# Optimization experiments

Hardware: AMD Instinct MI355X
Metric: run time of the kernel (lower is better)

Reference implementation:

```python
import jax, jax.numpy as jnp
import numpy as np

D_MODEL = 512
N_HEADS = 8
D_K = D_MODEL // N_HEADS  # 64
MAX_LEN = 5000


def _positional_encoding(d_model, max_len):
    pe = np.zeros((max_len, d_model), dtype=np.float32)
    position = np.arange(max_len, dtype=np.float32)[:, None]
    div_term = np.exp(np.arange(0, d_model, 2, dtype=np.float32) * (-np.log(10000.0) / d_model))
    pe[:, 0::2] = np.sin(position * div_term)
    pe[:, 1::2] = np.cos(position * div_term)
    return jnp.asarray(pe)


def _layer_norm(x, gamma, beta, eps):
    mu = jnp.mean(x, axis=-1, keepdims=True)
    var = jnp.mean(jnp.square(x - mu), axis=-1, keepdims=True)
    return (x - mu) * jax.lax.rsqrt(var + eps) * gamma + beta


def setup_inputs() -> dict:
    key = jax.random.key(0)
    ks = jax.random.split(key, 5)
    s = 1.0 / np.sqrt(D_MODEL)
    return {
        "x": jax.random.normal(ks[0], (4, 2048, D_MODEL), dtype=jnp.float32),
        "ln1_g": jnp.ones((D_MODEL,), jnp.float32),
        "ln1_b": jnp.zeros((D_MODEL,), jnp.float32),
        "wq": jax.random.normal(ks[1], (D_MODEL, D_MODEL), jnp.float32) * s,
        "wk": jax.random.normal(ks[2], (D_MODEL, D_MODEL), jnp.float32) * s,
        "wv": jax.random.normal(ks[3], (D_MODEL, D_MODEL), jnp.float32) * s,
        "wfc": jax.random.normal(ks[4], (D_MODEL, D_MODEL), jnp.float32) * s,
        "ln2_g": jnp.ones((D_MODEL,), jnp.float32),
        "ln2_b": jnp.zeros((D_MODEL,), jnp.float32),
    }


def reference(x, ln1_g, ln1_b, wq, wk, wv, wfc, ln2_g, ln2_b):
    B, T, D = x.shape
    residual0 = x
    # outer pre-norm (nn.LayerNorm default eps=1e-5)
    h = _layer_norm(x, ln1_g, ln1_b, 1e-5)
    # sinusoidal positional encoding
    h = h + _positional_encoding(D_MODEL, MAX_LEN)[:T]
    residual1 = h
    # projections -> [B, H, T, d]
    q = (h @ wq).reshape(B, T, N_HEADS, D_K).transpose(0, 2, 1, 3)
    k = (h @ wk).reshape(B, T, N_HEADS, D_K).transpose(0, 2, 1, 3)
    v = (h @ wv).reshape(B, T, N_HEADS, D_K).transpose(0, 2, 1, 3)
    scale = 1.0 / np.sqrt(D_K).astype(np.float32)
    attn = jnp.einsum("bhqd,bhkd->bhqk", q * scale, k)
    causal = jnp.tril(jnp.ones((T, T), dtype=bool))  # subsequent mask
    attn = jnp.where(causal, attn, jnp.float32(-1e9))
    attn = jax.nn.softmax(attn, axis=-1)
    o = jnp.einsum("bhqk,bhkd->bhqd", attn, v)
    o = o.transpose(0, 2, 1, 3).reshape(B, T, D)
    o = o @ wfc
    # inner post-attention residual + LayerNorm (eps=1e-6)
    h2 = _layer_norm(o + residual1, ln2_g, ln2_b, 1e-6)
    return h2 + residual0
```

## Files before the change

kernel.cpp:

```cpp
#include <hip/hip_runtime.h>
#include <hip/hip_bf16.h>

#define B_ 4
#define T_ 2048
#define D_ 512

typedef __attribute__((ext_vector_type(8))) short short8;
typedef __attribute__((ext_vector_type(4))) short short4v;
typedef __attribute__((ext_vector_type(4))) float float4v;
typedef unsigned short bf16_t;

__device__ __forceinline__ bf16_t f2bf(float f) {
  unsigned int u = __builtin_bit_cast(unsigned int, f);
  unsigned int r = (u + 0x7fffu + ((u >> 16) & 1u)) >> 16;
  return (bf16_t)r;
}

__device__ __forceinline__ float waveReduceSum(float v) {
#pragma unroll
  for (int m = 32; m >= 1; m >>= 1) v += __shfl_xor(v, m, 64);
  return v;
}

__device__ __forceinline__ void gld16(const bf16_t* g, bf16_t* l) {
  __builtin_amdgcn_global_load_lds(
      (const __attribute__((address_space(1))) void*)g,
      (__attribute__((address_space(3))) void*)l, 16, 0, 0);
}

__global__ __launch_bounds__(256) void wconv_kernel(
    const float* __restrict__ wq, const float* __restrict__ wk,
    const float* __restrict__ wv, const float* __restrict__ wfc,
    bf16_t* __restrict__ wqkvT, bf16_t* __restrict__ wfcT) {
  for (int idx = blockIdx.x * 256 + threadIdx.x; idx < 1048576; idx += 262144) {
    if (idx < 786432) {
      int n = idx >> 9, k = idx & 511;
      const float* src = (n < 512) ? wq : ((n < 1024) ? wk : wv);
      float scl = (n >= 512 && n < 1024) ? 0.125f : 1.0f;
      int c = n & 511;
      wqkvT[idx] = f2bf(src[k * 512 + c] * scl);
    } else {
      int j = idx - 786432;
      int n = j >> 9, k = j & 511;
      wfcT[j] = f2bf(wfc[k * 512 + n]);
    }
  }
}

__global__ __launch_bounds__(256) void ln1_pe_kernel(
    const float* __restrict__ x, const float* __restrict__ g,
    const float* __restrict__ bb, float* __restrict__ h_f32,
    bf16_t* __restrict__ h_bf16) {
  int wave = threadIdx.x >> 6, lane = threadIdx.x & 63;
  int row = blockIdx.x * 4 + wave;
  int pos = row & (T_ - 1);
  const float* xr = x + (size_t)row * D_;
  int c0 = lane * 8;
  float v[8];
  float4 a = *(const float4*)(xr + c0);
  float4 b4 = *(const float4*)(xr + c0 + 4);
  v[0]=a.x; v[1]=a.y; v[2]=a.z; v[3]=a.w;
  v[4]=b4.x; v[5]=b4.y; v[6]=b4.z; v[7]=b4.w;
  float s = 0.f;
#pragma unroll
  for (int j = 0; j < 8; ++j) s += v[j];
  s = waveReduceSum(s);
  float mu = s * (1.f / 512.f);
  float q = 0.f;
#pragma unroll
  for (int j = 0; j < 8; ++j) { float d = v[j] - mu; q += d * d; }
  q = waveReduceSum(q);
  float rstd = rsqrtf(q * (1.f / 512.f) + 1e-5f);
  float* hr = h_f32 + (size_t)row * D_;
  bf16_t* hb = h_bf16 + (size_t)row * D_;
#pragma unroll
  for (int j = 0; j < 8; ++j) {
    int col = c0 + j;
    float hn = (v[j] - mu) * rstd * g[col] + bb[col];
    int i2 = (col >> 1) << 1;
    float dt = __expf((float)i2 * (-9.2103403719761836f / 512.0f));
    float ang = (float)pos * dt;
    float pe = (col & 1) ? __cosf(ang) : __sinf(ang);
    float hv = hn + pe;
    hr[col] = hv;
    hb[col] = f2bf(hv);
  }
}

template <int N_COLS, int OUT_BF16>
__global__ __launch_bounds__(256) void gemm128_kernel(
    const bf16_t* __restrict__ A, const bf16_t* __restrict__ Bt,
    void* __restrict__ Cv) {
  __shared__ __align__(16) bf16_t As[128 * 64];
  __shared__ __align__(16) bf16_t Bs[128 * 64];
  const int m0 = blockIdx.y * 128, n0 = blockIdx.x * 128;
  const int tid = threadIdx.x;
  const int w = tid >> 6, lane = tid & 63;
  const int ln = lane & 15, quad = lane >> 4;
  const int wy = w >> 1, wx = w & 1;
  const int sw = ln & 7;

  float4v acc[4][4];
  float4v z = {0.f, 0.f, 0.f, 0.f};
#pragma unroll
  for (int i = 0; i < 4; ++i)
#pragma unroll
    for (int j = 0; j < 4; ++j) acc[i][j] = z;

  for (int k0 = 0; k0 < 512; k0 += 64) {
#pragma unroll
    for (int i = 0; i < 4; ++i) {
      int cbase = w * 256 + i * 64;
      int chunk = cbase + lane;
      int row = chunk >> 3;
      int lb = (chunk & 7) ^ (row & 7);
      gld16(A + (size_t)(m0 + row) * 512 + k0 + lb * 8, As + (size_t)cbase * 8);
      gld16(Bt + (size_t)(n0 + row) * 512 + k0 + lb * 8, Bs + (size_t)cbase * 8);
    }
    __syncthreads();
#pragma unroll
    for (int c = 0; c < 2; ++c) {
      short8 af[4], bf[4];
#pragma unroll
      for (int mt = 0; mt < 4; ++mt) {
        int row = wy * 64 + mt * 16 + ln;
        int pb = (c * 4 + quad) ^ sw;
        af[mt] = *(const short8*)(As + row * 64 + pb * 8);
      }
#pragma unroll
      for (int nt = 0; nt < 4; ++nt) {
        int row = wx * 64 + nt * 16 + ln;
        int pb = (c * 4 + quad) ^ sw;
        bf[nt] = *(const short8*)(Bs + row * 64 + pb * 8);
      }
#pragma unroll
      for (int mt = 0; mt < 4; ++mt)
#pragma unroll
        for (int nt = 0; nt < 4; ++nt)
          acc[mt][nt] = __builtin_amdgcn_mfma_f32_16x16x32_bf16(af[mt], bf[nt], acc[mt][nt], 0, 0, 0);
    }
    __syncthreads();
  }
#pragma unroll
  for (int mt = 0; mt < 4; ++mt)
#pragma unroll
    for (int r = 0; r < 4; ++r) {
      int row = m0 + wy * 64 + mt * 16 + quad * 4 + r;
#pragma unroll
      for (int nt = 0; nt < 4; ++nt) {
        int col = n0 + wx * 64 + nt * 16 + ln;
        if (OUT_BF16)
          ((bf16_t*)Cv)[(size_t)row * N_COLS + col] = f2bf(acc[mt][nt][r]);
        else
          ((float*)Cv)[(size_t)row * N_COLS + col] = acc[mt][nt][r];
      }
    }
}

__global__ __launch_bounds__(256) void attn_kernel(const bf16_t* __restrict__ qk,
                                                   const bf16_t* __restrict__ vT,
                                                   bf16_t* __restrict__ out) {
  __shared__ __align__(16) bf16_t Ks[2][64 * 64];
  __shared__ __align__(16) bf16_t Vs[2][64 * 64];
  __shared__ __align__(16) bf16_t Ps[4][16 * 72];
  const int bx = blockIdx.x;
  const int qt = 31 - (bx >> 5);
  const int bh = bx & 31;
  const int b = bh >> 3, h = bh & 7;
  const int tid = threadIdx.x;
  const int w = tid >> 6, lane = tid & 63;
  const int ln = lane & 15, quad = lane >> 4;
  const int sw = ln & 7;

  short8 qf0, qf1;
  {
    size_t qrow = ((size_t)b * T_ + qt * 64 + w * 16 + ln) * 1024 + h * 64;
    qf0 = *(const short8*)(qk + qrow + quad * 8);
    qf1 = *(const short8*)(qk + qrow + 32 + quad * 8);
  }
  float4v z = {0.f, 0.f, 0.f, 0.f};
  float4v oacc[4];
#pragma unroll
  for (int i = 0; i < 4; ++i) oacc[i] = z;
  float m_s = -1e30f, l_s = 0.f;

  const bf16_t* kbase = qk + (size_t)b * T_ * 1024 + 512 + h * 64;
  const bf16_t* vbase = vT + (size_t)(h * 64) * 8192 + (size_t)b * T_;
  bf16_t* Psw = Ps[w];

  auto stage = [&](int buf, int kt) {
#pragma unroll
    for (int i = 0; i < 2; ++i) {
      int cbase = w * 128 + i * 64;
      int chunk = cbase + lane;
      int row = chunk >> 3;
      int lb = (chunk & 7) ^ (row & 7);
      gld16(kbase + (size_t)(kt * 64 + row) * 1024 + lb * 8, Ks[buf] + (size_t)cbase * 8);
      gld16(vbase + (size_t)row * 8192 + kt * 64 + lb * 8, Vs[buf] + (size_t)cbase * 8);
    }
  };

  auto compute = [&](const bf16_t* Kc, const bf16_t* Vc, bool mask) {
    float sv[4][4];
#pragma unroll
    for (int mt = 0; mt < 4; ++mt) {
      float4v st = z;
      int row = mt * 16 + ln;
      short8 a0 = *(const short8*)(Kc + row * 64 + ((0 + quad) ^ sw) * 8);
      short8 a1 = *(const short8*)(Kc + row * 64 + ((4 + quad) ^ sw) * 8);
      st = __builtin_amdgcn_mfma_f32_16x16x32_bf16(a0, qf0, st, 0, 0, 0);
      st = __builtin_amdgcn_mfma_f32_16x16x32_bf16(a1, qf1, st, 0, 0, 0);
#pragma unroll
      for (int r = 0; r < 4; ++r) {
        float v = st[r];
        if (mask) {
          int kloc = mt * 16 + quad * 4 + r;
          if (kloc > w * 16 + ln) v = -1e30f;
        }
        sv[mt][r] = v;
      }
    }
    float mx = sv[0][0];
#pragma unroll
    for (int mt = 0; mt < 4; ++mt)
#pragma unroll
      for (int r = 0; r < 4; ++r) mx = fmaxf(mx, sv[mt][r]);
    mx = fmaxf(mx, __shfl_xor(mx, 16, 64));
    mx = fmaxf(mx, __shfl_xor(mx, 32, 64));
    float mn = fmaxf(m_s, mx);
    float alpha = __expf(m_s - mn);
    m_s = mn;
    float rs = 0.f;
#pragma unroll
    for (int mt = 0; mt < 4; ++mt)
#pragma unroll
      for (int r = 0; r < 4; ++r) {
        float p = __expf(sv[mt][r] - mn);
        sv[mt][r] = p;
        rs += p;
      }
    rs += __shfl_xor(rs, 16, 64);
    rs += __shfl_xor(rs, 32, 64);
    l_s = l_s * alpha + rs;
#pragma unroll
    for (int dt = 0; dt < 4; ++dt)
#pragma unroll
      for (int r = 0; r < 4; ++r) oacc[dt][r] *= alpha;
#pragma unroll
    for (int mt = 0; mt < 4; ++mt) {
      short4v p4;
#pragma unroll
      for (int r = 0; r < 4; ++r) p4[r] = (short)f2bf(sv[mt][r]);
      *(short4v*)(Psw + ln * 72 + mt * 16 + quad * 4) = p4;
    }
    short8 bp0 = *(short8*)(Psw + ln * 72 + quad * 8);
    short8 bp1 = *(short8*)(Psw + ln * 72 + 32 + quad * 8);
#pragma unroll
    for (int dt = 0; dt < 4; ++dt) {
      int row = dt * 16 + ln;
      short8 av0 = *(const short8*)(Vc + row * 64 + ((0 + quad) ^ sw) * 8);
      short8 av1 = *(const short8*)(Vc + row * 64 + ((4 + quad) ^ sw) * 8);
      oacc[dt] = __builtin_amdgcn_mfma_f32_16x16x32_bf16(av0, bp0, oacc[dt], 0, 0, 0);
      oacc[dt] = __builtin_amdgcn_mfma_f32_16x16x32_bf16(av1, bp1, oacc[dt], 0, 0, 0);
    }
  };

  stage(0, 0);
  __syncthreads();
  for (int kt = 0; kt < qt; ++kt) {
    int cur = kt & 1;
    stage(cur ^ 1, kt + 1);
    compute(Ks[cur], Vs[cur], false);
    __syncthreads();
  }
  compute(Ks[qt & 1], Vs[qt & 1], true);

  float inv = 1.0f / l_s;
  size_t obase = ((size_t)b * T_ + qt * 64 + w * 16 + ln) * 512 + h * 64;
#pragma unroll
  for (int dt = 0; dt < 4; ++dt) {
    short4v o4;
#pragma unroll
    for (int r = 0; r < 4; ++r) o4[r] = (short)f2bf(oacc[dt][r] * inv);
    *(short4v*)(out + obase + dt * 16 + quad * 4) = o4;
  }
}

__global__ __launch_bounds__(256) void ln2_kernel(
    const float* __restrict__ o2, const float* __restrict__ hres,
    const float* __restrict__ x, const float* __restrict__ g,
    const float* __restrict__ bb, float* __restrict__ out) {
  int wave = threadIdx.x >> 6, lane = threadIdx.x & 63;
  int row = blockIdx.x * 4 + wave;
  size_t ro = (size_t)row * D_;
  int c0 = lane * 8;
  float t[8];
  float4 a0 = *(const float4*)(o2 + ro + c0);
  float4 a1 = *(const float4*)(o2 + ro + c0 + 4);
  float4 h0 = *(const float4*)(hres + ro + c0);
  float4 h1 = *(const float4*)(hres + ro + c0 + 4);
  t[0]=a0.x+h0.x; t[1]=a0.y+h0.y; t[2]=a0.z+h0.z; t[3]=a0.w+h0.w;
  t[4]=a1.x+h1.x; t[5]=a1.y+h1.y; t[6]=a1.z+h1.z; t[7]=a1.w+h1.w;
  float s = 0.f;
#pragma unroll
  for (int j = 0; j < 8; ++j) s += t[j];
  s = waveReduceSum(s);
  float mu = s * (1.f / 512.f);
  float q = 0.f;
#pragma unroll
  for (int j = 0; j < 8; ++j) { float d = t[j] - mu; q += d * d; }
  q = waveReduceSum(q);
  float rstd = rsqrtf(q * (1.f / 512.f) + 1e-6f);
#pragma unroll
  for (int j = 0; j < 8; ++j) {
    int col = c0 + j;
    out[ro + col] = (t[j] - mu) * rstd * g[col] + bb[col] + x[ro + col];
  }
}

extern "C" void kernel_launch(void* const* d_in, const int* in_sizes, int n_in,
                              void* d_out, int out_size, void* d_ws, size_t ws_size,
                              hipStream_t stream) {
  const float* x   = (const float*)d_in[0];
  const float* g1  = (const float*)d_in[1];
  const float* b1  = (const float*)d_in[2];
  const float* wq  = (const float*)d_in[3];
  const float* wk  = (const float*)d_in[4];
  const float* wv  = (const float*)d_in[5];
  const float* wfc = (const float*)d_in[6];
  const float* g2  = (const float*)d_in[7];
  const float* b2  = (const float*)d_in[8];
  float* out = (float*)d_out;

  char* ws = (char*)d_ws;
  const size_t O_HF32  = 0;
  const size_t O_HBF   = 16777216;
  const size_t O_WQKV  = 25165824;
  const size_t O_WFC   = 26738688;
  const size_t O_QK    = 27262976;
  const size_t O_VT    = 44040192;
  const size_t O_ATTN  = 52428800;
  const size_t O_O2    = 60817408;
  const size_t WS_NEED = 77594624;
  if (ws_size < WS_NEED) return;

  float*  h_f32 = (float*)(ws + O_HF32);
  bf16_t* h_bf  = (bf16_t*)(ws + O_HBF);
  bf16_t* wqkvT = (bf16_t*)(ws + O_WQKV);
  bf16_t* wfcT  = (bf16_t*)(ws + O_WFC);
  bf16_t* qk    = (bf16_t*)(ws + O_QK);
  bf16_t* vT    = (bf16_t*)(ws + O_VT);
  bf16_t* attn  = (bf16_t*)(ws + O_ATTN);
  float*  o2    = (float*)(ws + O_O2);

  wconv_kernel<<<dim3(1024), dim3(256), 0, stream>>>(wq, wk, wv, wfc, wqkvT, wfcT);
  ln1_pe_kernel<<<dim3(2048), dim3(256), 0, stream>>>(x, g1, b1, h_f32, h_bf);
  gemm128_kernel<1024, 1><<<dim3(8, 64), dim3(256), 0, stream>>>(h_bf, wqkvT, (void*)qk);
  gemm128_kernel<8192, 1><<<dim3(64, 4), dim3(256), 0, stream>>>(wqkvT + 1024 * 512, h_bf, (void*)vT);
  attn_kernel<<<dim3(1024), dim3(256), 0, stream>>>(qk, vT, attn);
  gemm128_kernel<512, 0><<<dim3(4, 64), dim3(256), 0, stream>>>(attn, wfcT, (void*)o2);
  ln2_kernel<<<dim3(2048), dim3(256), 0, stream>>>(o2, h_f32, x, g2, b2, out);
}
```

Measured before the change: 196.9 us.

## Fuse prep kernels, double-buffer GEMMs, merge QKV launches, fold residual into GEMM epilogue

Result: no change. 196.0 us (-0.5%).

```diff
diff --git a/kernel.cpp b/kernel.cpp
--- a/kernel.cpp
+++ b/kernel.cpp
@@ -15,6 +15,10 @@
   unsigned int r = (u + 0x7fffu + ((u >> 16) & 1u)) >> 16;
   return (bf16_t)r;
 }
+__device__ __forceinline__ float bf2f(bf16_t b) {
+  unsigned int u = ((unsigned int)b) << 16;
+  return __builtin_bit_cast(float, u);
+}
 
 __device__ __forceinline__ float waveReduceSum(float v) {
 #pragma unroll
@@ -28,29 +32,32 @@
       (__attribute__((address_space(3))) void*)l, 16, 0, 0);
 }
 
-__global__ __launch_bounds__(256) void wconv_kernel(
+__global__ __launch_bounds__(256) void pre_kernel(
+    const float* __restrict__ x, const float* __restrict__ g,
+    const float* __restrict__ bb,
     const float* __restrict__ wq, const float* __restrict__ wk,
     const float* __restrict__ wv, const float* __restrict__ wfc,
+    bf16_t* __restrict__ h_bf16,
     bf16_t* __restrict__ wqkvT, bf16_t* __restrict__ wfcT) {
-  for (int idx = blockIdx.x * 256 + threadIdx.x; idx < 1048576; idx += 262144) {
-    if (idx < 786432) {
-      int n = idx >> 9, k = idx & 511;
-      const float* src = (n < 512) ? wq : ((n < 1024) ? wk : wv);
-      float scl = (n >= 512 && n < 1024) ? 0.125f : 1.0f;
-      int c = n & 511;
-      wqkvT[idx] = f2bf(src[k * 512 + c] * scl);
-    } else {
-      int j = idx - 786432;
-      int n = j >> 9, k = j & 511;
-      wfcT[j] = f2bf(wfc[k * 512 + n]);
-    }
-  }
-}
-
-__global__ __launch_bounds__(256) void ln1_pe_kernel(
-    const float* __restrict__ x, const float* __restrict__ g,
-    const float* __restrict__ bb, float* __restrict__ h_f32,
-    bf16_t* __restrict__ h_bf16) {
+  if (blockIdx.x >= 2048) {
+    int bid = blockIdx.x - 2048;
+#pragma unroll 4
+    for (int i = 0; i < 16; ++i) {
+      int idx = bid * 4096 + i * 256 + threadIdx.x;
+      if (idx < 786432) {
+        int n = idx >> 9, k = idx & 511;
+        const float* src = (n < 512) ? wq : ((n < 1024) ? wk : wv);
+        float scl = (n >= 512 && n < 1024) ? 0.125f : 1.0f;
+        int c = n & 511;
+        wqkvT[idx] = f2bf(src[k * 512 + c] * scl);
+      } else {
+        int j = idx - 786432;
+        int n = j >> 9, k = j & 511;
+        wfcT[j] = f2bf(wfc[k * 512 + n]);
+      }
+    }
+    return;
+  }
   int wave = threadIdx.x >> 6, lane = threadIdx.x & 63;
   int row = blockIdx.x * 4 + wave;
   int pos = row & (T_ - 1);
@@ -71,7 +78,6 @@
   for (int j = 0; j < 8; ++j) { float d = v[j] - mu; q += d * d; }
   q = waveReduceSum(q);
   float rstd = rsqrtf(q * (1.f / 512.f) + 1e-5f);
-  float* hr = h_f32 + (size_t)row * D_;
   bf16_t* hb = h_bf16 + (size_t)row * D_;
 #pragma unroll
   for (int j = 0; j < 8; ++j) {
@@ -81,19 +87,15 @@
     float dt = __expf((float)i2 * (-9.2103403719761836f / 512.0f));
     float ang = (float)pos * dt;
     float pe = (col & 1) ? __cosf(ang) : __sinf(ang);
-    float hv = hn + pe;
-    hr[col] = hv;
-    hb[col] = f2bf(hv);
-  }
-}
-
-template <int N_COLS, int OUT_BF16>
-__global__ __launch_bounds__(256) void gemm128_kernel(
-    const bf16_t* __restrict__ A, const bf16_t* __restrict__ Bt,
-    void* __restrict__ Cv) {
-  __shared__ __align__(16) bf16_t As[128 * 64];
-  __shared__ __align__(16) bf16_t Bs[128 * 64];
-  const int m0 = blockIdx.y * 128, n0 = blockIdx.x * 128;
+    hb[col] = f2bf(hn + pe);
+  }
+}
+
+template <typename EPI>
+__device__ __forceinline__ void gemm_body(const bf16_t* __restrict__ A,
+                                          const bf16_t* __restrict__ Bt,
+                                          int m0, int n0, bf16_t* As, bf16_t* Bs,
+                                          EPI epi) {
   const int tid = threadIdx.x;
   const int w = tid >> 6, lane = tid & 63;
   const int ln = lane & 15, quad = lane >> 4;
@@ -107,32 +109,34 @@
 #pragma unroll
     for (int j = 0; j < 4; ++j) acc[i][j] = z;
 
-  for (int k0 = 0; k0 < 512; k0 += 64) {
+  auto stage = [&](int buf, int k0) {
 #pragma unroll
     for (int i = 0; i < 4; ++i) {
       int cbase = w * 256 + i * 64;
       int chunk = cbase + lane;
       int row = chunk >> 3;
       int lb = (chunk & 7) ^ (row & 7);
-      gld16(A + (size_t)(m0 + row) * 512 + k0 + lb * 8, As + (size_t)cbase * 8);
-      gld16(Bt + (size_t)(n0 + row) * 512 + k0 + lb * 8, Bs + (size_t)cbase * 8);
-    }
-    __syncthreads();
+      gld16(A + (size_t)(m0 + row) * 512 + k0 + lb * 8, As + buf * 8192 + cbase * 8);
+      gld16(Bt + (size_t)(n0 + row) * 512 + k0 + lb * 8, Bs + buf * 8192 + cbase * 8);
+    }
+  };
+
+  stage(0, 0);
+  __syncthreads();
+  for (int kb = 0; kb < 8; ++kb) {
+    int cur = kb & 1;
+    if (kb < 7) stage(cur ^ 1, (kb + 1) * 64);
+    const bf16_t* Ac = As + cur * 8192;
+    const bf16_t* Bc = Bs + cur * 8192;
 #pragma unroll
     for (int c = 0; c < 2; ++c) {
       short8 af[4], bf[4];
 #pragma unroll
-      for (int mt = 0; mt < 4; ++mt) {
-        int row = wy * 64 + mt * 16 + ln;
-        int pb = (c * 4 + quad) ^ sw;
-        af[mt] = *(const short8*)(As + row * 64 + pb * 8);
-      }
-#pragma unroll
-      for (int nt = 0; nt < 4; ++nt) {
-        int row = wx * 64 + nt * 16 + ln;
-        int pb = (c * 4 + quad) ^ sw;
-        bf[nt] = *(const short8*)(Bs + row * 64 + pb * 8);
-      }
+      for (int mt = 0; mt < 4; ++mt)
+        af[mt] = *(const short8*)(Ac + (wy * 64 + mt * 16 + ln) * 64 + (((c * 4 + quad) ^ sw)) * 8);
+#pragma unroll
+      for (int nt = 0; nt < 4; ++nt)
+        bf[nt] = *(const short8*)(Bc + (wx * 64 + nt * 16 + ln) * 64 + (((c * 4 + quad) ^ sw)) * 8);
 #pragma unroll
       for (int mt = 0; mt < 4; ++mt)
 #pragma unroll
@@ -149,12 +153,40 @@
 #pragma unroll
       for (int nt = 0; nt < 4; ++nt) {
         int col = n0 + wx * 64 + nt * 16 + ln;
-        if (OUT_BF16)
-          ((bf16_t*)Cv)[(size_t)row * N_COLS + col] = f2bf(acc[mt][nt][r]);
-        else
-          ((float*)Cv)[(size_t)row * N_COLS + col] = acc[mt][nt][r];
+        epi(row, col, acc[mt][nt][r]);
       }
     }
+}
+
+__global__ __launch_bounds__(256) void gemm_qkvt_kernel(
+    const bf16_t* __restrict__ h_bf, const bf16_t* __restrict__ wqkvT,
+    bf16_t* __restrict__ qk, bf16_t* __restrict__ vT) {
+  __shared__ __align__(16) bf16_t As[2 * 128 * 64];
+  __shared__ __align__(16) bf16_t Bs[2 * 128 * 64];
+  int bx = blockIdx.x;
+  if (bx < 512) {
+    int m0 = (bx >> 3) * 128, n0 = (bx & 7) * 128;
+    gemm_body(h_bf, wqkvT, m0, n0, As, Bs,
+              [&](int row, int col, float v) { qk[(size_t)row * 1024 + col] = f2bf(v); });
+  } else {
+    int local = bx - 512;
+    int m0 = (local >> 6) * 128, n0 = (local & 63) * 128;
+    gemm_body(wqkvT + 1024 * 512, h_bf, m0, n0, As, Bs,
+              [&](int row, int col, float v) { vT[(size_t)row * 8192 + col] = f2bf(v); });
+  }
+}
+
+__global__ __launch_bounds__(256) void gemm_out_kernel(
+    const bf16_t* __restrict__ attn, const bf16_t* __restrict__ wfcT,
+    const bf16_t* __restrict__ h_bf, bf16_t* __restrict__ o2r) {
+  __shared__ __align__(16) bf16_t As[2 * 128 * 64];
+  __shared__ __align__(16) bf16_t Bs[2 * 128 * 64];
+  int bx = blockIdx.x;
+  int m0 = (bx >> 2) * 128, n0 = (bx & 3) * 128;
+  gemm_body(attn, wfcT, m0, n0, As, Bs, [&](int row, int col, float v) {
+    size_t o = (size_t)row * 512 + col;
+    o2r[o] = f2bf(v + bf2f(h_bf[o]));
+  });
 }
 
 __global__ __launch_bounds__(256) void attn_kernel(const bf16_t* __restrict__ qk,
@@ -287,20 +319,17 @@
 }
 
 __global__ __launch_bounds__(256) void ln2_kernel(
-    const float* __restrict__ o2, const float* __restrict__ hres,
-    const float* __restrict__ x, const float* __restrict__ g,
-    const float* __restrict__ bb, float* __restrict__ out) {
+    const bf16_t* __restrict__ o2r, const float* __restrict__ x,
+    const float* __restrict__ g, const float* __restrict__ bb,
+    float* __restrict__ out) {
   int wave = threadIdx.x >> 6, lane = threadIdx.x & 63;
   int row = blockIdx.x * 4 + wave;
   size_t ro = (size_t)row * D_;
   int c0 = lane * 8;
+  short8 ov = *(const short8*)(o2r + ro + c0);
   float t[8];
-  float4 a0 = *(const float4*)(o2 + ro + c0);
-  float4 a1 = *(const float4*)(o2 + ro + c0 + 4);
-  float4 h0 = *(const float4*)(hres + ro + c0);
-  float4 h1 = *(const float4*)(hres + ro + c0 + 4);
-  t[0]=a0.x+h0.x; t[1]=a0.y+h0.y; t[2]=a0.z+h0.z; t[3]=a0.w+h0.w;
-  t[4]=a1.x+h1.x; t[5]=a1.y+h1.y; t[6]=a1.z+h1.z; t[7]=a1.w+h1.w;
+#pragma unroll
+  for (int j = 0; j < 8; ++j) t[j] = bf2f((bf16_t)ov[j]);
   float s = 0.f;
 #pragma unroll
   for (int j = 0; j < 8; ++j) s += t[j];
@@ -311,11 +340,19 @@
   for (int j = 0; j < 8; ++j) { float d = t[j] - mu; q += d * d; }
   q = waveReduceSum(q);
   float rstd = rsqrtf(q * (1.f / 512.f) + 1e-6f);
+  float4 x0 = *(const float4*)(x + ro + c0);
+  float4 x1 = *(const float4*)(x + ro + c0 + 4);
+  float xr[8] = {x0.x, x0.y, x0.z, x0.w, x1.x, x1.y, x1.z, x1.w};
+  float o[8];
 #pragma unroll
   for (int j = 0; j < 8; ++j) {
     int col = c0 + j;
-    out[ro + col] = (t[j] - mu) * rstd * g[col] + bb[col] + x[ro + col];
-  }
+    o[j] = (t[j] - mu) * rstd * g[col] + bb[col] + xr[j];
+  }
+  float4 w0 = {o[0], o[1], o[2], o[3]};
+  float4 w1 = {o[4], o[5], o[6], o[7]};
+  *(float4*)(out + ro + c0) = w0;
+  *(float4*)(out + ro + c0 + 4) = w1;
 }
 
 extern "C" void kernel_launch(void* const* d_in, const int* in_sizes, int n_in,
@@ -333,31 +370,28 @@
   float* out = (float*)d_out;
 
   char* ws = (char*)d_ws;
-  const size_t O_HF32  = 0;
-  const size_t O_HBF   = 16777216;
-  const size_t O_WQKV  = 25165824;
-  const size_t O_WFC   = 26738688;
-  const size_t O_QK    = 27262976;
-  const size_t O_VT    = 44040192;
-  const size_t O_ATTN  = 52428800;
-  const size_t O_O2    = 60817408;
-  const size_t WS_NEED = 77594624;
+  const size_t O_HBF  = 0;
+  const size_t O_WQKV = 8388608;
+  const size_t O_WFC  = 9961472;
+  const size_t O_QK   = 10485760;
+  const size_t O_VT   = 27262976;
+  const size_t O_ATTN = 35651584;
+  const size_t O_O2R  = 44040192;
+  const size_t WS_NEED = 52428800;
   if (ws_size < WS_NEED) return;
 
-  float*  h_f32 = (float*)(ws + O_HF32);
   bf16_t* h_bf  = (bf16_t*)(ws + O_HBF);
   bf16_t* wqkvT = (bf16_t*)(ws + O_WQKV);
   bf16_t* wfcT  = (bf16_t*)(ws + O_WFC);
   bf16_t* qk    = (bf16_t*)(ws + O_QK);
   bf16_t* vT    = (bf16_t*)(ws + O_VT);
   bf16_t* attn  = (bf16_t*)(ws + O_ATTN);
-  float*  o2    = (float*)(ws + O_O2);
-
-  wconv_kernel<<<dim3(1024), dim3(256), 0, stream>>>(wq, wk, wv, wfc, wqkvT, wfcT);
-  ln1_pe_kernel<<<dim3(2048), dim3(256), 0, stream>>>(x, g1, b1, h_f32, h_bf);
-  gemm128_kernel<1024, 1><<<dim3(8, 64), dim3(256), 0, stream>>>(h_bf, wqkvT, (void*)qk);
-  gemm128_kernel<8192, 1><<<dim3(64, 4), dim3(256), 0, stream>>>(wqkvT + 1024 * 512, h_bf, (void*)vT);
+  bf16_t* o2r   = (bf16_t*)(ws + O_O2R);
+
+  pre_kernel<<<dim3(2304), dim3(256), 0, stream>>>(x, g1, b1, wq, wk, wv, wfc,
+                                                   h_bf, wqkvT, wfcT);
+  gemm_qkvt_kernel<<<dim3(768), dim3(256), 0, stream>>>(h_bf, wqkvT, qk, vT);
   attn_kernel<<<dim3(1024), dim3(256), 0, stream>>>(qk, vT, attn);
-  gemm128_kernel<512, 0><<<dim3(4, 64), dim3(256), 0, stream>>>(attn, wfcT, (void*)o2);
-  ln2_kernel<<<dim3(2048), dim3(256), 0, stream>>>(o2, h_f32, x, g2, b2, out);
-}
+  gemm_out_kernel<<<dim3(256), dim3(256), 0, stream>>>(attn, wfcT, h_bf, o2r);
+  ln2_kernel<<<dim3(2048), dim3(256), 0, stream>>>(o2r, x, g2, b2, out);
+}
```
